# Optimization experiments

Measured on AMD Instinct MI355X. Metric: run time of the kernel, lower is better.

## Reference

```python
import jax, jax.numpy as jnp
import numpy as np

N_NODES, F_IN, HID, HEADS, REP, NCLS = 8192, 128, 64, 8, 512, 32
E, NSYN, LMAX = 2048, 4096, 8
DM, DI, DSTATE, DCONV, DTR = 512, 1024, 16, 4, 32


def setup_inputs():
    key = jax.random.key(0)
    ks = jax.random.split(key, 24)
    g = lambda i, shape, s=0.05: jax.random.normal(ks[i], shape, jnp.float32) * s
    return {
        "edge_attr": jax.random.normal(ks[0], (E, 8), jnp.float32),
        "synapse": jax.random.normal(ks[1], (NSYN, 6), jnp.float32),
        "x_param": g(2, (N_NODES, F_IN), 0.1),
        "W1": g(3, (F_IN, HEADS * HID)),
        "att_src1": g(4, (HEADS, HID), 0.1),
        "att_dst1": g(5, (HEADS, HID), 0.1),
        "b1": jnp.zeros((HEADS * HID,), jnp.float32),
        "W2": g(6, (HEADS * HID, REP)),
        "att_src2": g(7, (1, REP), 0.1),
        "att_dst2": g(8, (1, REP), 0.1),
        "b2": jnp.zeros((REP,), jnp.float32),
        "W_in": g(9, (6, DM), 0.1),
        "b_in": jnp.zeros((DM,), jnp.float32),
        "W_inproj": g(10, (DM, 2 * DI)),
        "conv_w": g(11, (DI, DCONV), 0.1),
        "conv_b": jnp.zeros((DI,), jnp.float32),
        "W_xproj": g(12, (DI, DTR + 2 * DSTATE)),
        "W_dt": g(13, (DTR, DI), 0.1),
        "b_dt": jnp.full((DI,), -4.0, jnp.float32),
        "A_log": jnp.log(jnp.tile(jnp.arange(1, DSTATE + 1, dtype=jnp.float32), (DI, 1))),
        "D": jnp.ones((DI,), jnp.float32),
        "W_outproj": g(14, (DI, DM)),
        "W_lout": g(15, (DM, DM)),
        "b_lout": jnp.zeros((DM,), jnp.float32),
        "Wc1": g(16, (REP + 2 * DM, 512)),
        "bc1": jnp.zeros((512,), jnp.float32),
        "Wc2": g(17, (512, NCLS)),
        "bc2": jnp.zeros((NCLS,), jnp.float32),
        "edge_index": jax.random.randint(ks[18], (2, E), 0, N_NODES),
        "synapse_index": jnp.sort(jax.random.randint(ks[19], (NSYN,), 0, E)),
        "scatter_size": N_NODES,
    }


def _gat(x, W, a_src, a_dst, bias, src, dst, heads, out_ch, concat):
    # PyG GATConv (eval mode, edge_dim=None, self-loops already appended to src/dst)
    n = x.shape[0]
    xw = (x @ W).reshape(n, heads, out_ch)
    e = (xw * a_src).sum(-1)[src] + (xw * a_dst).sum(-1)[dst]  # [E+N, H]
    e = jax.nn.leaky_relu(e, 0.2)
    m = jax.ops.segment_max(e, dst, num_segments=n)
    ex = jnp.exp(e - m[dst])
    denom = jax.ops.segment_sum(ex, dst, num_segments=n)
    alpha = ex / denom[dst]
    out = jax.ops.segment_sum(alpha[:, :, None] * xw[src], dst, num_segments=n)
    out = out.reshape(n, heads * out_ch) if concat else out.mean(1)
    return out + bias


def _mamba_encoder(synapse, synapse_index, W_in, b_in, W_inproj, conv_w, conv_b,
                   W_xproj, W_dt, b_dt, A_log, D, W_outproj, W_lout, b_lout):
    # ragged [NSYN,6] -> padded [E, LMAX, 6] (synapse_index is sorted)
    counts = jax.ops.segment_sum(jnp.ones((NSYN,), jnp.int32), synapse_index, num_segments=E)
    starts = jnp.cumsum(counts) - counts
    pos = jnp.arange(NSYN) - starts[synapse_index]
    padded = jnp.zeros((E, LMAX, synapse.shape[1]), synapse.dtype).at[
        synapse_index, pos].set(synapse, mode="drop")
    u = padded @ W_in + b_in                     # linear_in: [E, L, DM]
    xz = u @ W_inproj                            # in_proj:   [E, L, 2*DI]
    xm, z = xz[..., :DI], xz[..., DI:]
    # depthwise causal conv over time
    xc = jax.lax.conv_general_dilated(
        xm.transpose(0, 2, 1), conv_w[:, None, :],
        window_strides=(1,), padding=[(DCONV - 1, 0)],
        dimension_numbers=("NCH", "OIH", "NCH"), feature_group_count=DI)
    xc = jax.nn.silu(xc + conv_b[:, None]).transpose(0, 2, 1)  # [E, L, DI]
    xdb = xc @ W_xproj
    dt = jax.nn.softplus(xdb[..., :DTR] @ W_dt + b_dt)         # [E, L, DI]
    Bm = xdb[..., DTR:DTR + DSTATE]                            # [E, L, N]
    Cm = xdb[..., DTR + DSTATE:]                               # [E, L, N]
    A = -jnp.exp(A_log)                                        # [DI, N]

    def step(h, t):
        dt_t, B_t, C_t, x_t = t                                # [E,DI],[E,N],[E,N],[E,DI]
        h = jnp.exp(dt_t[:, :, None] * A) * h + (dt_t * x_t)[:, :, None] * B_t[:, None, :]
        return h, jnp.einsum("bdn,bn->bd", h, C_t)

    h0 = jnp.zeros((E, DI, DSTATE), xc.dtype)
    _, ys = jax.lax.scan(step, h0, (dt.transpose(1, 0, 2), Bm.transpose(1, 0, 2),
                                    Cm.transpose(1, 0, 2), xc.transpose(1, 0, 2)))
    y = ys.transpose(1, 0, 2) + D * xc                         # [E, L, DI]
    out = (y * jax.nn.silu(z)) @ W_outproj                     # [E, L, DM]
    # masked mean over true sequence length (empty groups behave like a zero seq of len 1)
    cnt = jnp.clip(counts, 1, LMAX).astype(out.dtype)
    mask = (jnp.arange(LMAX)[None, :] < cnt[:, None]).astype(out.dtype)
    pooled = (out * mask[:, :, None]).sum(1) / cnt[:, None]
    return pooled @ W_lout + b_lout                            # [E, DM]


def _forward(edge_attr, synapse, x_param, W1, att_src1, att_dst1, b1,
             W2, att_src2, att_dst2, b2, W_in, b_in, W_inproj, conv_w, conv_b,
             W_xproj, W_dt, b_dt, A_log, D, W_outproj, W_lout, b_lout,
             Wc1, bc1, Wc2, bc2, edge_index, synapse_index, scatter_size):
    # GAT stack (eval: dropouts identity; edge_attr unused since edge_dim=None)
    loops = jnp.arange(N_NODES)
    src = jnp.concatenate([edge_index[0], loops])
    dst = jnp.concatenate([edge_index[1], loops])
    h = jax.nn.elu(_gat(x_param, W1, att_src1, att_dst1, b1, src, dst, HEADS, HID, True))
    h = _gat(h, W2, att_src2, att_dst2, b2, src, dst, 1, REP, False)   # [N, REP]
    x_point = _mamba_encoder(synapse, synapse_index, W_in, b_in, W_inproj, conv_w,
                             conv_b, W_xproj, W_dt, b_dt, A_log, D, W_outproj,
                             W_lout, b_lout)                            # [E, DM]

    def smax(idx):
        s = jax.ops.segment_max(x_point, idx, num_segments=scatter_size)
        nz = jax.ops.segment_sum(jnp.ones((E,), jnp.int32), idx, num_segments=scatter_size)
        return jnp.where(nz[:, None] > 0, s, 0.0)  # torch_scatter: empty slots -> 0

    left, right = smax(edge_index[0]), smax(edge_index[1])
    feats = jnp.concatenate([h, left, right], axis=1)          # [N, REP+2*DM]
    return jax.nn.relu(feats @ Wc1 + bc1) @ Wc2 + bc2          # [N, NCLS]


def reference(edge_attr, synapse, x_param, W1, att_src1, att_dst1, b1,
              W2, att_src2, att_dst2, b2, W_in, b_in, W_inproj, conv_w, conv_b,
              W_xproj, W_dt, b_dt, A_log, D, W_outproj, W_lout, b_lout,
              Wc1, bc1, Wc2, bc2, edge_index, synapse_index, scatter_size):
    return _forward(edge_attr, synapse, x_param, W1, att_src1, att_dst1, b1,
                    W2, att_src2, att_dst2, b2, W_in, b_in, W_inproj, conv_w, conv_b,
                    W_xproj, W_dt, b_dt, A_log, D, W_outproj, W_lout, b_lout,
                    Wc1, bc1, Wc2, bc2, edge_index, synapse_index, scatter_size)
```

## Files before the change

kernel.cpp:

```cpp
#include <hip/hip_runtime.h>

#define N_NODES 8192
#define F_IN 128
#define HID 64
#define HEADS 8
#define REP 512
#define NCLS 32
#define E_EDGES 2048
#define NSYN 4096
#define LMAX 8
#define DM 512
#define DI 1024
#define DSTATE 16
#define DCONV 4
#define DTR 32
#define TOT_EDGES (E_EDGES + N_NODES)
#define ROWS (E_EDGES * LMAX)
#define MC_CAP 6144

typedef short bf16x8 __attribute__((ext_vector_type(8)));
typedef float f32x4 __attribute__((ext_vector_type(4)));

__device__ __forceinline__ unsigned mapf(float f) {
  unsigned u = __float_as_uint(f);
  return (u & 0x80000000u) ? ~u : (u | 0x80000000u);
}
__device__ __forceinline__ float unmapf(unsigned u) {
  return __uint_as_float((u & 0x80000000u) ? (u ^ 0x80000000u) : ~u);
}
__device__ __forceinline__ float sigmoidf_(float x) { return 1.0f / (1.0f + expf(-x)); }
__device__ __forceinline__ float softplusf_(float x) {
  return fmaxf(x, 0.0f) + log1pf(expf(-fabsf(x)));
}
__device__ __forceinline__ float fsig(float x) {
  return __builtin_amdgcn_rcpf(1.0f + __expf(-x));
}
__device__ __forceinline__ float fsoftplus(float x) {
  return fmaxf(x, 0.0f) + __logf(1.0f + __expf(-fabsf(x)));
}
__device__ __forceinline__ unsigned short f2bf(float f) {
  unsigned u = __float_as_uint(f);
  unsigned r = (u + 0x7FFFu + ((u >> 16) & 1u)) >> 16;
  return (unsigned short)r;
}
__device__ __forceinline__ float bf2f(unsigned short h) {
  return __uint_as_float(((unsigned)h) << 16);
}
__device__ __forceinline__ void split2(float x, unsigned short* hh, unsigned short* ll) {
  unsigned short h = f2bf(x);
  *hh = h;
  *ll = f2bf(x - bf2f(h));
}
__device__ __forceinline__ int lower_bound_dev(const int* __restrict__ arr, int n, int v) {
  int lo = 0, hi = n;
  while (lo < hi) { int mid = (lo + hi) >> 1; if (arr[mid] < v) lo = mid + 1; else hi = mid; }
  return lo;
}
__device__ __forceinline__ int src_of(const int* __restrict__ ei, int i) {
  return i < E_EDGES ? ei[i] : i - E_EDGES;
}
__device__ __forceinline__ int dst_of(const int* __restrict__ ei, int i) {
  return i < E_EDGES ? ei[E_EDGES + i] : i - E_EDGES;
}
__device__ __forceinline__ int clip_cnt(int c) { return c < 1 ? 1 : (c > LMAX ? LMAX : c); }

__global__ __launch_bounds__(256) void gemm_mfma(
    const unsigned short* __restrict__ Ah, const unsigned short* __restrict__ Al,
    const unsigned short* __restrict__ Bth, const unsigned short* __restrict__ Btl,
    float* __restrict__ C, int M, int N, int K,
    const float* __restrict__ bias, int act) {
  __shared__ __align__(16) unsigned short As[2][64][40];
  const int tid = threadIdx.x;
  const int w = tid >> 6;
  const int lane = tid & 63;
  const int brow = blockIdx.y * 64;
  const int bcol = blockIdx.x * 64;
  const int srow = tid >> 2;
  const int skc = tid & 3;
  const int r0 = lane & 15;
  const int kg = lane >> 4;
  f32x4 acc[4] = {};
  const size_t aoff = (size_t)(brow + srow) * K + skc * 8;
  const size_t boff = (size_t)(bcol + w * 16 + r0) * K + kg * 8;
  bf16x8 bh = *(const bf16x8*)(Bth + boff);
  bf16x8 bl = *(const bf16x8*)(Btl + boff);
  *(bf16x8*)(&As[0][srow][skc * 8]) = *(const bf16x8*)(Ah + aoff);
  *(bf16x8*)(&As[1][srow][skc * 8]) = *(const bf16x8*)(Al + aoff);
  __syncthreads();
  for (int kt = 0; kt < K; kt += 32) {
    const bool more = (kt + 32) < K;
    bf16x8 nAh, nAl, nbh, nbl;
    if (more) {
      nAh = *(const bf16x8*)(Ah + aoff + kt + 32);
      nAl = *(const bf16x8*)(Al + aoff + kt + 32);
      nbh = *(const bf16x8*)(Bth + boff + kt + 32);
      nbl = *(const bf16x8*)(Btl + boff + kt + 32);
    }
#pragma unroll
    for (int r = 0; r < 4; ++r) {
      bf16x8 ah = *(const bf16x8*)(&As[0][r * 16 + r0][kg * 8]);
      bf16x8 al = *(const bf16x8*)(&As[1][r * 16 + r0][kg * 8]);
      acc[r] = __builtin_amdgcn_mfma_f32_16x16x32_bf16(ah, bh, acc[r], 0, 0, 0);
      acc[r] = __builtin_amdgcn_mfma_f32_16x16x32_bf16(ah, bl, acc[r], 0, 0, 0);
      acc[r] = __builtin_amdgcn_mfma_f32_16x16x32_bf16(al, bh, acc[r], 0, 0, 0);
    }
    __syncthreads();
    if (more) {
      *(bf16x8*)(&As[0][srow][skc * 8]) = nAh;
      *(bf16x8*)(&As[1][srow][skc * 8]) = nAl;
      bh = nbh; bl = nbl;
    }
    __syncthreads();
  }
  const int col = bcol + w * 16 + r0;
  const float bb = bias ? bias[col] : 0.0f;
#pragma unroll
  for (int r = 0; r < 4; ++r) {
#pragma unroll
    for (int j = 0; j < 4; ++j) {
      int row = brow + r * 16 + kg * 4 + j;
      float v = acc[r][j] + bb;
      if (act == 1) v = fmaxf(v, 0.0f);
      C[(size_t)row * N + col] = v;
    }
  }
}

__global__ __launch_bounds__(256) void gemm_mfma2(
    const unsigned short* __restrict__ Ah, const unsigned short* __restrict__ Al,
    const unsigned short* __restrict__ Bth, const unsigned short* __restrict__ Btl,
    float* __restrict__ C, int M, int N, int K,
    const float* __restrict__ bias, int act) {
  __shared__ __align__(16) unsigned short As[2][128][40];
  __shared__ __align__(16) unsigned short Bs[2][128][40];
  const int tid = threadIdx.x;
  const int w = tid >> 6;
  const int lane = tid & 63;
  const int wr = w >> 1, wc = w & 1;
  const int mb = M >> 7;
  const int lin = blockIdx.x;
  const int bx = lin / mb;
  const int by = lin % mb;
  const int brow = by * 128;
  const int bcol = bx * 128;
  const int r0 = lane & 15;
  const int kg = lane >> 4;
  const int row0 = tid >> 2, kc0 = tid & 3;
  const int row1 = (tid + 256) >> 2, kc1 = (tid + 256) & 3;
  const size_t a0 = (size_t)(brow + row0) * K + kc0 * 8;
  const size_t a1 = (size_t)(brow + row1) * K + kc1 * 8;
  const size_t b0 = (size_t)(bcol + row0) * K + kc0 * 8;
  const size_t b1 = (size_t)(bcol + row1) * K + kc1 * 8;
  f32x4 acc[4][4] = {};
  {
    bf16x8 t0 = *(const bf16x8*)(Ah + a0), t1 = *(const bf16x8*)(Al + a0);
    bf16x8 t2 = *(const bf16x8*)(Bth + b0), t3 = *(const bf16x8*)(Btl + b0);
    bf16x8 t4 = *(const bf16x8*)(Ah + a1), t5 = *(const bf16x8*)(Al + a1);
    bf16x8 t6 = *(const bf16x8*)(Bth + b1), t7 = *(const bf16x8*)(Btl + b1);
    *(bf16x8*)(&As[0][row0][kc0 * 8]) = t0;
    *(bf16x8*)(&As[1][row0][kc0 * 8]) = t1;
    *(bf16x8*)(&Bs[0][row0][kc0 * 8]) = t2;
    *(bf16x8*)(&Bs[1][row0][kc0 * 8]) = t3;
    *(bf16x8*)(&As[0][row1][kc1 * 8]) = t4;
    *(bf16x8*)(&As[1][row1][kc1 * 8]) = t5;
    *(bf16x8*)(&Bs[0][row1][kc1 * 8]) = t6;
    *(bf16x8*)(&Bs[1][row1][kc1 * 8]) = t7;
  }
  __syncthreads();
  for (int kt = 0; kt < K; kt += 32) {
    const bool more = (kt + 32) < K;
    bf16x8 p0, p1, p2, p3, p4, p5, p6, p7;
    if (more) {
      p0 = *(const bf16x8*)(Ah + a0 + kt + 32);
      p1 = *(const bf16x8*)(Al + a0 + kt + 32);
      p2 = *(const bf16x8*)(Bth + b0 + kt + 32);
      p3 = *(const bf16x8*)(Btl + b0 + kt + 32);
      p4 = *(const bf16x8*)(Ah + a1 + kt + 32);
      p5 = *(const bf16x8*)(Al + a1 + kt + 32);
      p6 = *(const bf16x8*)(Bth + b1 + kt + 32);
      p7 = *(const bf16x8*)(Btl + b1 + kt + 32);
    }
    bf16x8 bhv[4], blv[4];
#pragma unroll
    for (int cf = 0; cf < 4; ++cf) {
      bhv[cf] = *(const bf16x8*)(&Bs[0][wc * 64 + cf * 16 + r0][kg * 8]);
      blv[cf] = *(const bf16x8*)(&Bs[1][wc * 64 + cf * 16 + r0][kg * 8]);
    }
#pragma unroll
    for (int rf = 0; rf < 4; ++rf) {
      bf16x8 ah = *(const bf16x8*)(&As[0][wr * 64 + rf * 16 + r0][kg * 8]);
      bf16x8 al = *(const bf16x8*)(&As[1][wr * 64 + rf * 16 + r0][kg * 8]);
#pragma unroll
      for (int cf = 0; cf < 4; ++cf) {
        acc[rf][cf] = __builtin_amdgcn_mfma_f32_16x16x32_bf16(ah, bhv[cf], acc[rf][cf], 0, 0, 0);
        acc[rf][cf] = __builtin_amdgcn_mfma_f32_16x16x32_bf16(ah, blv[cf], acc[rf][cf], 0, 0, 0);
        acc[rf][cf] = __builtin_amdgcn_mfma_f32_16x16x32_bf16(al, bhv[cf], acc[rf][cf], 0, 0, 0);
      }
    }
    __syncthreads();
    if (more) {
      *(bf16x8*)(&As[0][row0][kc0 * 8]) = p0;
      *(bf16x8*)(&As[1][row0][kc0 * 8]) = p1;
      *(bf16x8*)(&Bs[0][row0][kc0 * 8]) = p2;
      *(bf16x8*)(&Bs[1][row0][kc0 * 8]) = p3;
      *(bf16x8*)(&As[0][row1][kc1 * 8]) = p4;
      *(bf16x8*)(&As[1][row1][kc1 * 8]) = p5;
      *(bf16x8*)(&Bs[0][row1][kc1 * 8]) = p6;
      *(bf16x8*)(&Bs[1][row1][kc1 * 8]) = p7;
    }
    __syncthreads();
  }
#pragma unroll
  for (int rf = 0; rf < 4; ++rf)
#pragma unroll
    for (int cf = 0; cf < 4; ++cf) {
      int col = bcol + wc * 64 + cf * 16 + r0;
      float bb = bias ? bias[col] : 0.0f;
#pragma unroll
      for (int j = 0; j < 4; ++j) {
        int row = brow + wr * 64 + rf * 16 + kg * 4 + j;
        float v = acc[rf][cf][j] + bb;
        if (act == 1) v = fmaxf(v, 0.0f);
        C[(size_t)row * N + col] = v;
      }
    }
}

__global__ __launch_bounds__(256) void gemm_mfma_sk(
    const unsigned short* __restrict__ Ah, const unsigned short* __restrict__ Al,
    const unsigned short* __restrict__ Bth, const unsigned short* __restrict__ Btl,
    float* __restrict__ C, int M, int N, int K) {
  __shared__ __align__(16) unsigned short As[2][64][40];
  const int tid = threadIdx.x;
  const int w = tid >> 6;
  const int lane = tid & 63;
  const int brow = blockIdx.y * 64;
  const int bcol = blockIdx.x * 64;
  const int srow = tid >> 2;
  const int skc = tid & 3;
  const int r0 = lane & 15;
  const int kg = lane >> 4;
  const int kchunk = K / gridDim.z;
  const int k0 = blockIdx.z * kchunk;
  f32x4 acc[4] = {};
  const size_t aoff = (size_t)(brow + srow) * K;
  const size_t boff = (size_t)(bcol + w * 16 + r0) * K + kg * 8;
  for (int kt = k0; kt < k0 + kchunk; kt += 32) {
    bf16x8 bh = *(const bf16x8*)(Bth + boff + kt);
    bf16x8 bl = *(const bf16x8*)(Btl + boff + kt);
    *(bf16x8*)(&As[0][srow][skc * 8]) = *(const bf16x8*)(Ah + aoff + kt + skc * 8);
    *(bf16x8*)(&As[1][srow][skc * 8]) = *(const bf16x8*)(Al + aoff + kt + skc * 8);
    __syncthreads();
#pragma unroll
    for (int r = 0; r < 4; ++r) {
      bf16x8 ah = *(const bf16x8*)(&As[0][r * 16 + r0][kg * 8]);
      bf16x8 al = *(const bf16x8*)(&As[1][r * 16 + r0][kg * 8]);
      acc[r] = __builtin_amdgcn_mfma_f32_16x16x32_bf16(ah, bh, acc[r], 0, 0, 0);
      acc[r] = __builtin_amdgcn_mfma_f32_16x16x32_bf16(ah, bl, acc[r], 0, 0, 0);
      acc[r] = __builtin_amdgcn_mfma_f32_16x16x32_bf16(al, bh, acc[r], 0, 0, 0);
    }
    __syncthreads();
  }
  const int col = bcol + w * 16 + r0;
#pragma unroll
  for (int r = 0; r < 4; ++r) {
#pragma unroll
    for (int j = 0; j < 4; ++j) {
      int row = brow + r * 16 + kg * 4 + j;
      atomicAdd(&C[(size_t)row * N + col], acc[r][j]);
    }
  }
}

__global__ void split_kernel(const float* __restrict__ x, unsigned short* __restrict__ h,
                             unsigned short* __restrict__ l, int n) {
  int i = blockIdx.x * 256 + threadIdx.x;
  if (i >= n) return;
  split2(x[i], &h[i], &l[i]);
}

__global__ void tsplit_kernel(const float* __restrict__ W, unsigned short* __restrict__ Wth,
                              unsigned short* __restrict__ Wtl, int K, int N) {
  int i = blockIdx.x * 256 + threadIdx.x;
  if (i >= K * N) return;
  int k = i / N, n = i - k * N;
  float v = W[i];
  unsigned short h = f2bf(v);
  Wth[(size_t)n * K + k] = h;
  Wtl[(size_t)n * K + k] = f2bf(v - bf2f(h));
}

template <int BM, int BN>
__global__ __launch_bounds__(256) void gemm_t(
    const float* __restrict__ A, int lda,
    const float* __restrict__ B, int ldb,
    float* __restrict__ C, int ldc,
    int M, int N, int K,
    const float* __restrict__ bias, int act) {
  constexpr int RR = BM / 64;
  constexpr int CR = BN / 64;
  __shared__ float As[16][BM + 4];
  __shared__ float Bs[16][BN + 4];
  const int tid = threadIdx.x;
  const int tx = tid & 15;
  const int ty = tid >> 4;
  const int brow = blockIdx.y * BM;
  const int bcol = blockIdx.x * BN;
  float acc[RR][CR][4][4] = {};
  for (int kt = 0; kt < K; kt += 16) {
#pragma unroll
    for (int p = 0; p < RR; ++p) {
      int c = tid + p * 256;
      int row = c >> 2, kc = c & 3;
      int gr = brow + row;
      float4 v = make_float4(0.f, 0.f, 0.f, 0.f);
      if (gr < M) v = *reinterpret_cast<const float4*>(A + (size_t)gr * lda + kt + kc * 4);
      As[kc * 4 + 0][row] = v.x;
      As[kc * 4 + 1][row] = v.y;
      As[kc * 4 + 2][row] = v.z;
      As[kc * 4 + 3][row] = v.w;
    }
#pragma unroll
    for (int p = 0; p < CR; ++p) {
      int c = tid + p * 256;
      int k = c / (BN / 4), c4 = c % (BN / 4);
      int gc = bcol + c4 * 4;
      float4 v = make_float4(0.f, 0.f, 0.f, 0.f);
      if (gc < N) v = *reinterpret_cast<const float4*>(B + (size_t)(kt + k) * ldb + gc);
      *reinterpret_cast<float4*>(&Bs[k][c4 * 4]) = v;
    }
    __syncthreads();
#pragma unroll
    for (int k = 0; k < 16; ++k) {
      float av[RR * 4], bv[CR * 4];
#pragma unroll
      for (int r = 0; r < RR; ++r) {
        float4 t = *reinterpret_cast<const float4*>(&As[k][r * 64 + ty * 4]);
        av[r * 4 + 0] = t.x; av[r * 4 + 1] = t.y; av[r * 4 + 2] = t.z; av[r * 4 + 3] = t.w;
      }
#pragma unroll
      for (int cq = 0; cq < CR; ++cq) {
        float4 t = *reinterpret_cast<const float4*>(&Bs[k][cq * 64 + tx * 4]);
        bv[cq * 4 + 0] = t.x; bv[cq * 4 + 1] = t.y; bv[cq * 4 + 2] = t.z; bv[cq * 4 + 3] = t.w;
      }
#pragma unroll
      for (int r = 0; r < RR; ++r)
#pragma unroll
        for (int cq = 0; cq < CR; ++cq)
#pragma unroll
          for (int i = 0; i < 4; ++i)
#pragma unroll
            for (int j = 0; j < 4; ++j)
              acc[r][cq][i][j] = fmaf(av[r * 4 + i], bv[cq * 4 + j], acc[r][cq][i][j]);
    }
    __syncthreads();
  }
#pragma unroll
  for (int r = 0; r < RR; ++r)
#pragma unroll
    for (int i = 0; i < 4; ++i) {
      int row = brow + r * 64 + ty * 4 + i;
      if (row >= M) continue;
#pragma unroll
      for (int cq = 0; cq < CR; ++cq) {
        int col = bcol + cq * 64 + tx * 4;
        if (col >= N) continue;
        float4 v;
        v.x = acc[r][cq][i][0]; v.y = acc[r][cq][i][1];
        v.z = acc[r][cq][i][2]; v.w = acc[r][cq][i][3];
        if (bias) {
          float4 bb = *reinterpret_cast<const float4*>(bias + col);
          v.x += bb.x; v.y += bb.y; v.z += bb.z; v.w += bb.w;
        }
        if (act == 1) {
          v.x = fmaxf(v.x, 0.f); v.y = fmaxf(v.y, 0.f);
          v.z = fmaxf(v.z, 0.f); v.w = fmaxf(v.w, 0.f);
        }
        *reinterpret_cast<float4*>(C + (size_t)row * ldc + col) = v;
      }
    }
}

__global__ void counts_kernel(const int* __restrict__ sidx, int* __restrict__ counts) {
  int e = blockIdx.x * 256 + threadIdx.x;
  if (e >= E_EDGES) return;
  int lo = lower_bound_dev(sidx, NSYN, e);
  int hi = lower_bound_dev(sidx, NSYN, e + 1);
  counts[e] = hi - lo;
}

__global__ void scatter_padded_kernel(const float* __restrict__ synapse,
                                      const int* __restrict__ sidx,
                                      float* __restrict__ padded) {
  int i = blockIdx.x * 256 + threadIdx.x;
  if (i >= NSYN) return;
  int e = sidx[i];
  int lo = lower_bound_dev(sidx, NSYN, e);
  int pos = i - lo;
  if (pos < LMAX) {
#pragma unroll
    for (int c = 0; c < 6; ++c) padded[((size_t)e * LMAX + pos) * 6 + c] = synapse[(size_t)i * 6 + c];
  }
}

__global__ __launch_bounds__(256) void prefix_kernel(const int* __restrict__ counts,
                                                     int* __restrict__ starts_c) {
  __shared__ int part[256];
  int t = threadIdx.x;
  int loc[8];
  int s = 0;
#pragma unroll
  for (int i = 0; i < 8; ++i) {
    int c = clip_cnt(counts[t * 8 + i]);
    loc[i] = s;
    s += c;
  }
  part[t] = s;
  __syncthreads();
  int mytot = s;
  for (int o = 1; o < 256; o <<= 1) {
    int add = (t >= o) ? part[t - o] : 0;
    __syncthreads();
    part[t] += add;
    __syncthreads();
  }
  int off = part[t] - mytot;
#pragma unroll
  for (int i = 0; i < 8; ++i) starts_c[t * 8 + i] = off + loc[i];
}

__global__ __launch_bounds__(256) void xc_compact_kernel(
    const float* __restrict__ padded,
    const float* __restrict__ W_eff, const float* __restrict__ b_eff,
    const float* __restrict__ conv_w, const float* __restrict__ conv_b,
    const int* __restrict__ counts, const int* __restrict__ starts_c,
    unsigned short* __restrict__ xch, unsigned short* __restrict__ xcl) {
  __shared__ float pads[LMAX * 6];
  int t = threadIdx.x;
  int d = blockIdx.x * 256 + t;
  int e = blockIdx.y;
  if (t < LMAX * 6) pads[t] = padded[(size_t)e * LMAX * 6 + t];
  __syncthreads();
  int cnt = clip_cnt(counts[e]);
  int sc = starts_c[e];
  float wef[6];
#pragma unroll
  for (int c = 0; c < 6; ++c) wef[c] = W_eff[c * 2048 + d];
  float cw0 = conv_w[d * 4 + 0], cw1 = conv_w[d * 4 + 1];
  float cw2 = conv_w[d * 4 + 2], cw3 = conv_w[d * 4 + 3];
  float cb = conv_b[d], be = b_eff[d];
  float x0 = 0.f, x1 = 0.f, x2 = 0.f;
  for (int l = 0; l < cnt; ++l) {
    float xm = be;
#pragma unroll
    for (int c = 0; c < 6; ++c) xm += pads[l * 6 + c] * wef[c];
    float s0 = cb + xm * cw3;
    if (l >= 1) s0 += x2 * cw2;
    if (l >= 2) s0 += x1 * cw1;
    if (l >= 3) s0 += x0 * cw0;
    float v = s0 * fsig(s0);
    size_t o = (size_t)(sc + l) * DI + d;
    split2(v, &xch[o], &xcl[o]);
    x0 = x1; x1 = x2; x2 = xm;
  }
}

__global__ __launch_bounds__(256) void mamba_scan_pool_kernel(
    const float* __restrict__ xdb_c, const float* __restrict__ padded,
    const float* __restrict__ W_eff, const float* __restrict__ b_eff,
    const float* __restrict__ W_dt, const float* __restrict__ b_dt,
    const float* __restrict__ A_log, const float* __restrict__ Dv,
    const float* __restrict__ conv_w, const float* __restrict__ conv_b,
    const int* __restrict__ counts, const int* __restrict__ starts_c,
    unsigned short* __restrict__ pooledh, unsigned short* __restrict__ pooledl) {
  __shared__ float pads[LMAX * 6];
  int t = threadIdx.x;
  int d = blockIdx.x * 256 + t;
  int e = blockIdx.y;
  if (t < LMAX * 6) pads[t] = padded[(size_t)e * LMAX * 6 + t];
  float wdt[DTR];
#pragma unroll
  for (int k = 0; k < DTR; ++k) wdt[k] = W_dt[k * DI + d];
  float a[DSTATE];
#pragma unroll
  for (int n = 0; n < DSTATE; ++n) a[n] = -__expf(A_log[d * DSTATE + n]);
  float h[DSTATE];
#pragma unroll
  for (int n = 0; n < DSTATE; ++n) h[n] = 0.0f;
  float wef[6], wez[6];
#pragma unroll
  for (int c = 0; c < 6; ++c) {
    wef[c] = W_eff[c * 2048 + d];
    wez[c] = W_eff[c * 2048 + DI + d];
  }
  float cw0 = conv_w[d * 4 + 0], cw1 = conv_w[d * 4 + 1];
  float cw2 = conv_w[d * 4 + 2], cw3 = conv_w[d * 4 + 3];
  float cb = conv_b[d];
  float bdt = b_dt[d], Dd = Dv[d], be = b_eff[d], bez = b_eff[DI + d];
  __syncthreads();
  int cnt = clip_cnt(counts[e]);
  int sc = starts_c[e];
  float x0 = 0.f, x1 = 0.f, x2 = 0.f;
  float ssum = 0.0f;
  for (int l = 0; l < cnt; ++l) {
    float xm = be;
#pragma unroll
    for (int c = 0; c < 6; ++c) xm += pads[l * 6 + c] * wef[c];
    float s0 = cb + xm * cw3;
    if (l >= 1) s0 += x2 * cw2;
    if (l >= 2) s0 += x1 * cw1;
    if (l >= 3) s0 += x0 * cw0;
    float xt = s0 * fsig(s0);
    const float* __restrict__ xrow = xdb_c + (size_t)(sc + l) * 64;
    float acc = bdt;
#pragma unroll
    for (int k = 0; k < DTR; ++k) acc += xrow[k] * wdt[k];
    float dt = fsoftplus(acc);
    float dtx = dt * xt;
    float y = 0.0f;
#pragma unroll
    for (int n = 0; n < DSTATE; ++n) {
      float en = __expf(dt * a[n]);
      h[n] = en * h[n] + dtx * xrow[32 + n];
      y += h[n] * xrow[48 + n];
    }
    y += Dd * xt;
    float z = bez;
#pragma unroll
    for (int c = 0; c < 6; ++c) z += pads[l * 6 + c] * wez[c];
    ssum += y * z * fsig(z);
    x0 = x1; x1 = x2; x2 = xm;
  }
  float pv = ssum / (float)cnt;
  split2(pv, &pooledh[(size_t)e * DI + d], &pooledl[(size_t)e * DI + d]);
}

__global__ void esed1_kernel(const float* __restrict__ xw1, const float* __restrict__ as1,
                             const float* __restrict__ ad1, float* __restrict__ es1,
                             float* __restrict__ ed1) {
  int idx = blockIdx.x * 256 + threadIdx.x;
  int n = idx >> 3, h = idx & 7;
  const float* xr = xw1 + (size_t)n * 512 + h * 64;
  const float* sr = as1 + h * 64;
  const float* dr = ad1 + h * 64;
  float es = 0.0f, ed = 0.0f;
#pragma unroll
  for (int c = 0; c < 64; ++c) { float v = xr[c]; es += v * sr[c]; ed += v * dr[c]; }
  es1[idx] = es; ed1[idx] = ed;
}

__global__ void edge1_kernel(const int* __restrict__ ei, const float* __restrict__ es1,
                             const float* __restrict__ ed1, float* __restrict__ e1,
                             unsigned* __restrict__ m1u) {
  int idx = blockIdx.x * 256 + threadIdx.x;
  if (idx >= TOT_EDGES * HEADS) return;
  int i = idx >> 3, h = idx & 7;
  int s = src_of(ei, i), d = dst_of(ei, i);
  float v = es1[s * 8 + h] + ed1[d * 8 + h];
  v = v >= 0.0f ? v : 0.2f * v;
  e1[idx] = v;
  atomicMax(m1u + d * 8 + h, mapf(v));
}

__global__ void ex1_kernel(const int* __restrict__ ei, float* __restrict__ e1,
                           const unsigned* __restrict__ m1u, float* __restrict__ denom1) {
  int idx = blockIdx.x * 256 + threadIdx.x;
  if (idx >= TOT_EDGES * HEADS) return;
  int i = idx >> 3, h = idx & 7;
  int d = dst_of(ei, i);
  float ex = expf(e1[idx] - unmapf(m1u[d * 8 + h]));
  e1[idx] = ex;
  atomicAdd(denom1 + d * 8 + h, ex);
}

__global__ __launch_bounds__(256) void agg1_kernel(const int* __restrict__ ei,
                                                   const float* __restrict__ e1,
                                                   const float* __restrict__ denom1,
                                                   const float* __restrict__ xw1,
                                                   float* __restrict__ g1) {
  int i = blockIdx.x;
  int s = src_of(ei, i), d = dst_of(ei, i);
  for (int j = threadIdx.x; j < 512; j += 256) {
    int h = j >> 6;
    float alpha = e1[i * 8 + h] / denom1[d * 8 + h];
    atomicAdd(g1 + (size_t)d * 512 + j, alpha * xw1[(size_t)s * 512 + j]);
  }
}

__global__ void elu_bias_split_kernel(const float* __restrict__ g1, const float* __restrict__ b1,
                                      unsigned short* __restrict__ g1h,
                                      unsigned short* __restrict__ g1l) {
  int idx = blockIdx.x * 256 + threadIdx.x;
  int j = idx & 511;
  float v = g1[idx] + b1[j];
  v = v > 0.0f ? v : expm1f(v);
  split2(v, &g1h[idx], &g1l[idx]);
}

__global__ __launch_bounds__(64) void esed2_kernel(const float* __restrict__ xw2,
                                                   const float* __restrict__ as2,
                                                   const float* __restrict__ ad2,
                                                   float* __restrict__ es2,
                                                   float* __restrict__ ed2) {
  int n = blockIdx.x, t = threadIdx.x;
  float es = 0.0f, ed = 0.0f;
  for (int c = t; c < 512; c += 64) {
    float v = xw2[(size_t)n * 512 + c];
    es += v * as2[c]; ed += v * ad2[c];
  }
#pragma unroll
  for (int o = 32; o > 0; o >>= 1) { es += __shfl_down(es, o, 64); ed += __shfl_down(ed, o, 64); }
  if (t == 0) { es2[n] = es; ed2[n] = ed; }
}

__global__ void edge2_kernel(const int* __restrict__ ei, const float* __restrict__ es2,
                             const float* __restrict__ ed2, float* __restrict__ e2,
                             unsigned* __restrict__ m2u) {
  int i = blockIdx.x * 256 + threadIdx.x;
  if (i >= TOT_EDGES) return;
  int s = src_of(ei, i), d = dst_of(ei, i);
  float v = es2[s] + ed2[d];
  v = v >= 0.0f ? v : 0.2f * v;
  e2[i] = v;
  atomicMax(m2u + d, mapf(v));
}

__global__ void ex2_kernel(const int* __restrict__ ei, float* __restrict__ e2,
                           const unsigned* __restrict__ m2u, float* __restrict__ denom2) {
  int i = blockIdx.x * 256 + threadIdx.x;
  if (i >= TOT_EDGES) return;
  int d = dst_of(ei, i);
  float ex = expf(e2[i] - unmapf(m2u[d]));
  e2[i] = ex;
  atomicAdd(denom2 + d, ex);
}

__global__ __launch_bounds__(256) void agg2_kernel(const int* __restrict__ ei,
                                                   const float* __restrict__ e2,
                                                   const float* __restrict__ denom2,
                                                   const float* __restrict__ xw2,
                                                   float* __restrict__ g2) {
  int i = blockIdx.x;
  int s = src_of(ei, i), d = dst_of(ei, i);
  float alpha = e2[i] / denom2[d];
  for (int j = threadIdx.x; j < 512; j += 256) {
    atomicAdd(g2 + (size_t)d * 512 + j, alpha * xw2[(size_t)s * 512 + j]);
  }
}

__global__ __launch_bounds__(256) void leftright_kernel(const int* __restrict__ ei,
                                                        const float* __restrict__ xp,
                                                        unsigned* __restrict__ leftU,
                                                        unsigned* __restrict__ rightU,
                                                        int* __restrict__ flagL,
                                                        int* __restrict__ flagR) {
  int i = blockIdx.x;
  int s = ei[i], d = ei[E_EDGES + i];
  if (threadIdx.x == 0) { flagL[s] = 1; flagR[d] = 1; }
  for (int j = threadIdx.x; j < 512; j += 256) {
    unsigned v = mapf(xp[(size_t)i * 512 + j]);
    atomicMax(leftU + (size_t)s * 512 + j, v);
    atomicMax(rightU + (size_t)d * 512 + j, v);
  }
}

__global__ void concat_split_kernel(const float* __restrict__ g2, const float* __restrict__ b2,
                                    const unsigned* __restrict__ leftU,
                                    const unsigned* __restrict__ rightU,
                                    const int* __restrict__ flagL, const int* __restrict__ flagR,
                                    unsigned short* __restrict__ fh,
                                    unsigned short* __restrict__ fl) {
  int idx = blockIdx.x * 256 + threadIdx.x;
  int n = idx >> 9, j = idx & 511;
  size_t base = (size_t)n * 1536 + j;
  split2(g2[idx] + b2[j], &fh[base], &fl[base]);
  split2(flagL[n] ? unmapf(leftU[idx]) : 0.0f, &fh[base + 512], &fl[base + 512]);
  split2(flagR[n] ? unmapf(rightU[idx]) : 0.0f, &fh[base + 1024], &fl[base + 1024]);
}

extern "C" void kernel_launch(void* const* d_in, const int* in_sizes, int n_in,
                              void* d_out, int out_size, void* d_ws, size_t ws_size,
                              hipStream_t stream) {
  const float* synapse = (const float*)d_in[1];
  const float* x_param = (const float*)d_in[2];
  const float* W1 = (const float*)d_in[3];
  const float* as1 = (const float*)d_in[4];
  const float* ad1 = (const float*)d_in[5];
  const float* b1 = (const float*)d_in[6];
  const float* W2 = (const float*)d_in[7];
  const float* as2 = (const float*)d_in[8];
  const float* ad2 = (const float*)d_in[9];
  const float* b2 = (const float*)d_in[10];
  const float* W_in = (const float*)d_in[11];
  const float* b_in = (const float*)d_in[12];
  const float* W_inproj = (const float*)d_in[13];
  const float* conv_w = (const float*)d_in[14];
  const float* conv_b = (const float*)d_in[15];
  const float* W_xproj = (const float*)d_in[16];
  const float* W_dt = (const float*)d_in[17];
  const float* b_dt = (const float*)d_in[18];
  const float* A_log = (const float*)d_in[19];
  const float* Dv = (const float*)d_in[20];
  const float* W_outproj = (const float*)d_in[21];
  const float* W_lout = (const float*)d_in[22];
  const float* b_lout = (const float*)d_in[23];
  const float* Wc1 = (const float*)d_in[24];
  const float* bc1 = (const float*)d_in[25];
  const float* Wc2 = (const float*)d_in[26];
  const float* bc2 = (const float*)d_in[27];
  const int* edge_index = (const int*)d_in[28];
  const int* sidx = (const int*)d_in[29];
  float* out = (float*)d_out;

  const size_t MB = (size_t)1 << 20;
  const size_t KB = (size_t)1 << 10;
  char* ws = (char*)d_ws;
  unsigned short* xc_ch = (unsigned short*)(ws + 0);
  unsigned short* xc_cl = (unsigned short*)(ws + 16 * MB);
  float* xw1 = (float*)(ws + 0);
  float* g1 = (float*)(ws + 16 * MB);
  unsigned short* g1h = (unsigned short*)(ws + 32 * MB);
  unsigned short* g1l = (unsigned short*)(ws + 40 * MB);
  unsigned short* xph = (unsigned short*)(ws + 48 * MB);
  unsigned short* xpl = (unsigned short*)(ws + 50 * MB);
  unsigned short* W1th = (unsigned short*)(ws + 52 * MB);
  unsigned short* W1tl = (unsigned short*)(ws + 52 * MB + 128 * KB);
  float* xw2 = (float*)(ws + 48 * MB);
  unsigned short* W2th = (unsigned short*)(ws + 0);
  unsigned short* W2tl = (unsigned short*)(ws + 512 * KB);
  float* g2 = (float*)(ws + 0);
  unsigned short* featsh = (unsigned short*)(ws + 16 * MB);
  unsigned short* featsl = (unsigned short*)(ws + 40 * MB);
  float* hidden = (float*)(ws + 0);
  float* xdb_c = (float*)(ws + 64 * MB);
  unsigned short* pooledh = (unsigned short*)(ws + 68 * MB);
  unsigned short* pooledl = (unsigned short*)(ws + 72 * MB);
  unsigned short* Wxth = (unsigned short*)(ws + 76 * MB);
  unsigned short* Wxtl = (unsigned short*)(ws + 76 * MB + 128 * KB);
  float* Wmix = (float*)(ws + 77 * MB);
  unsigned short* Wmixth = (unsigned short*)(ws + 80 * MB);
  unsigned short* Wmixtl = (unsigned short*)(ws + 81 * MB);
  unsigned* leftU = (unsigned*)(ws + 64 * MB);
  unsigned* rightU = (unsigned*)(ws + 80 * MB);
  float* x_point = (float*)(ws + 96 * MB);
  unsigned short* Wc1th = (unsigned short*)(ws + 96 * MB);
  unsigned short* Wc1tl = (unsigned short*)(ws + 96 * MB + 1536 * KB);
  char* sm = ws + 100 * MB;
  float* es1 = (float*)(sm + 0);
  float* ed1 = (float*)(sm + 256 * KB);
  float* e1 = (float*)(sm + 512 * KB);
  unsigned* m1u = (unsigned*)(sm + 832 * KB);
  float* denom1 = (float*)(sm + 1088 * KB);
  float* es2 = (float*)(sm + 1344 * KB);
  float* ed2 = (float*)(sm + 1376 * KB);
  float* e2 = (float*)(sm + 1408 * KB);
  unsigned* m2u = (unsigned*)(sm + 1448 * KB);
  float* denom2 = (float*)(sm + 1480 * KB);
  int* flagL = (int*)(sm + 1512 * KB);
  int* flagR = (int*)(sm + 1544 * KB);
  float* padded = (float*)(ws + 106 * MB);
  int* counts = (int*)(ws + 106 * MB + 384 * KB);
  float* W_eff = (float*)(ws + 106 * MB + 400 * KB);
  float* b_eff = (float*)(ws + 106 * MB + 448 * KB);
  int* starts_c = (int*)(ws + 106 * MB + 456 * KB);

  auto g64 = [&](const float* A, int lda, const float* B, int ldb, float* C, int ldc,
                 int M, int N, int K, const float* bias, int act) {
    dim3 grid((N + 63) / 64, (M + 63) / 64);
    gemm_t<64, 64><<<grid, 256, 0, stream>>>(A, lda, B, ldb, C, ldc, M, N, K, bias, act);
  };
  auto gm = [&](const unsigned short* Ah, const unsigned short* Al,
                const unsigned short* Bth, const unsigned short* Btl, float* C,
                int M, int N, int K, const float* bias, int act) {
    dim3 grid(N / 64, M / 64);
    gemm_mfma<<<grid, 256, 0, stream>>>(Ah, Al, Bth, Btl, C, M, N, K, bias, act);
  };
  auto gm2 = [&](const unsigned short* Ah, const unsigned short* Al,
                 const unsigned short* Bth, const unsigned short* Btl, float* C,
                 int M, int N, int K, const float* bias, int act) {
    gemm_mfma2<<<(N / 128) * (M / 128), 256, 0, stream>>>(Ah, Al, Bth, Btl, C, M, N, K, bias,
                                                          act);
  };
  auto tsplit = [&](const float* W, unsigned short* th, unsigned short* tl, int K, int N) {
    tsplit_kernel<<<(K * N + 255) / 256, 256, 0, stream>>>(W, th, tl, K, N);
  };

  g64(W_in, DM, W_inproj, 2 * DI, W_eff, 2 * DI, 6, 2 * DI, DM, nullptr, 0);
  g64(b_in, DM, W_inproj, 2 * DI, b_eff, 2 * DI, 1, 2 * DI, DM, nullptr, 0);
  g64(W_outproj, DM, W_lout, DM, Wmix, DM, DI, DM, DM, nullptr, 0);

  hipMemsetAsync(padded, 0, (size_t)ROWS * 6 * 4, stream);
  scatter_padded_kernel<<<(NSYN + 255) / 256, 256, 0, stream>>>(synapse, sidx, padded);
  counts_kernel<<<(E_EDGES + 255) / 256, 256, 0, stream>>>(sidx, counts);
  prefix_kernel<<<1, 256, 0, stream>>>(counts, starts_c);
  xc_compact_kernel<<<dim3(DI / 256, E_EDGES), 256, 0, stream>>>(
      padded, W_eff, b_eff, conv_w, conv_b, counts, starts_c, xc_ch, xc_cl);
  tsplit(W_xproj, Wxth, Wxtl, DI, 64);
  hipMemsetAsync(xdb_c, 0, (size_t)MC_CAP * 64 * 4, stream);
  gemm_mfma_sk<<<dim3(1, MC_CAP / 64, 8), 256, 0, stream>>>(xc_ch, xc_cl, Wxth, Wxtl, xdb_c,
                                                            MC_CAP, 64, DI);
  mamba_scan_pool_kernel<<<dim3(DI / 256, E_EDGES), 256, 0, stream>>>(
      xdb_c, padded, W_eff, b_eff, W_dt, b_dt, A_log, Dv, conv_w, conv_b, counts, starts_c,
      pooledh, pooledl);
  tsplit(Wmix, Wmixth, Wmixtl, DI, DM);
  gm(pooledh, pooledl, Wmixth, Wmixtl, x_point, E_EDGES, DM, DI, b_lout, 0);

  split_kernel<<<(N_NODES * F_IN + 255) / 256, 256, 0, stream>>>(x_param, xph, xpl,
                                                                 N_NODES * F_IN);
  tsplit(W1, W1th, W1tl, F_IN, HEADS * HID);
  gm2(xph, xpl, W1th, W1tl, xw1, N_NODES, HEADS * HID, F_IN, nullptr, 0);
  esed1_kernel<<<(N_NODES * HEADS) / 256, 256, 0, stream>>>(xw1, as1, ad1, es1, ed1);
  hipMemsetAsync(m1u, 0, 512 * KB, stream);
  hipMemsetAsync(g1, 0, (size_t)N_NODES * 512 * 4, stream);
  edge1_kernel<<<(TOT_EDGES * HEADS + 255) / 256, 256, 0, stream>>>(edge_index, es1, ed1, e1, m1u);
  ex1_kernel<<<(TOT_EDGES * HEADS + 255) / 256, 256, 0, stream>>>(edge_index, e1, m1u, denom1);
  agg1_kernel<<<TOT_EDGES, 256, 0, stream>>>(edge_index, e1, denom1, xw1, g1);
  elu_bias_split_kernel<<<(N_NODES * 512) / 256, 256, 0, stream>>>(g1, b1, g1h, g1l);

  tsplit(W2, W2th, W2tl, HEADS * HID, REP);
  gm2(g1h, g1l, W2th, W2tl, xw2, N_NODES, REP, HEADS * HID, nullptr, 0);
  esed2_kernel<<<N_NODES, 64, 0, stream>>>(xw2, as2, ad2, es2, ed2);
  hipMemsetAsync(m2u, 0, 128 * KB, stream);
  hipMemsetAsync(g2, 0, (size_t)N_NODES * 512 * 4, stream);
  edge2_kernel<<<(TOT_EDGES + 255) / 256, 256, 0, stream>>>(edge_index, es2, ed2, e2, m2u);
  ex2_kernel<<<(TOT_EDGES + 255) / 256, 256, 0, stream>>>(edge_index, e2, m2u, denom2);
  agg2_kernel<<<TOT_EDGES, 256, 0, stream>>>(edge_index, e2, denom2, xw2, g2);

  hipMemsetAsync(leftU, 0, 32 * MB, stream);
  leftright_kernel<<<E_EDGES, 256, 0, stream>>>(edge_index, x_point, leftU, rightU, flagL, flagR);

  concat_split_kernel<<<(N_NODES * 512) / 256, 256, 0, stream>>>(g2, b2, leftU, rightU, flagL,
                                                                 flagR, featsh, featsl);
  tsplit(Wc1, Wc1th, Wc1tl, REP + 2 * DM, 512);
  gm2(featsh, featsl, Wc1th, Wc1tl, hidden, N_NODES, 512, REP + 2 * DM, bc1, 1);
  g64(hidden, 512, Wc2, NCLS, out, NCLS, N_NODES, NCLS, 512, bc2, 0);
}
```

Baseline: 486.9 us.

## Replace GAT self-loop atomics with direct init kernels and widen GEMM to 512 threads

The GAT aggregation previously zeroed g1/g2 with a memset and then ran atomic scatter-adds over all edges plus one self-loop per node. Self-loop contributions are now written directly by an elementwise init kernel, so the memset and 8192 blocks of atomics per layer go away and only the real edges use atomicAdd. Separately, the 128x128 MFMA GEMM now runs with 512 threads: each of 8 waves computes a 64x32 sub-tile and each thread loads one chunk instead of two. This cuts per-thread registers and adds waves, at the cost of more LDS reads per MFMA.

```diff
diff --git a/kernel.cpp b/kernel.cpp
--- a/kernel.cpp
+++ b/kernel.cpp
@@ -27,10 +27,6 @@
 }
 __device__ __forceinline__ float unmapf(unsigned u) {
   return __uint_as_float((u & 0x80000000u) ? (u ^ 0x80000000u) : ~u);
-}
-__device__ __forceinline__ float sigmoidf_(float x) { return 1.0f / (1.0f + expf(-x)); }
-__device__ __forceinline__ float softplusf_(float x) {
-  return fmaxf(x, 0.0f) + log1pf(expf(-fabsf(x)));
 }
 __device__ __forceinline__ float fsig(float x) {
   return __builtin_amdgcn_rcpf(1.0f + __expf(-x));
@@ -126,7 +122,7 @@
   }
 }
 
-__global__ __launch_bounds__(256) void gemm_mfma2(
+__global__ __launch_bounds__(512) void gemm_mfma2(
     const unsigned short* __restrict__ Ah, const unsigned short* __restrict__ Al,
     const unsigned short* __restrict__ Bth, const unsigned short* __restrict__ Btl,
     float* __restrict__ C, int M, int N, int K,
@@ -136,7 +132,7 @@
   const int tid = threadIdx.x;
   const int w = tid >> 6;
   const int lane = tid & 63;
-  const int wr = w >> 1, wc = w & 1;
+  const int wr = w >> 2, wc = w & 3;
   const int mb = M >> 7;
   const int lin = blockIdx.x;
   const int bx = lin / mb;
@@ -146,52 +142,39 @@
   const int r0 = lane & 15;
   const int kg = lane >> 4;
   const int row0 = tid >> 2, kc0 = tid & 3;
-  const int row1 = (tid + 256) >> 2, kc1 = (tid + 256) & 3;
   const size_t a0 = (size_t)(brow + row0) * K + kc0 * 8;
-  const size_t a1 = (size_t)(brow + row1) * K + kc1 * 8;
   const size_t b0 = (size_t)(bcol + row0) * K + kc0 * 8;
-  const size_t b1 = (size_t)(bcol + row1) * K + kc1 * 8;
-  f32x4 acc[4][4] = {};
+  f32x4 acc[4][2] = {};
   {
     bf16x8 t0 = *(const bf16x8*)(Ah + a0), t1 = *(const bf16x8*)(Al + a0);
     bf16x8 t2 = *(const bf16x8*)(Bth + b0), t3 = *(const bf16x8*)(Btl + b0);
-    bf16x8 t4 = *(const bf16x8*)(Ah + a1), t5 = *(const bf16x8*)(Al + a1);
-    bf16x8 t6 = *(const bf16x8*)(Bth + b1), t7 = *(const bf16x8*)(Btl + b1);
     *(bf16x8*)(&As[0][row0][kc0 * 8]) = t0;
     *(bf16x8*)(&As[1][row0][kc0 * 8]) = t1;
     *(bf16x8*)(&Bs[0][row0][kc0 * 8]) = t2;
     *(bf16x8*)(&Bs[1][row0][kc0 * 8]) = t3;
-    *(bf16x8*)(&As[0][row1][kc1 * 8]) = t4;
-    *(bf16x8*)(&As[1][row1][kc1 * 8]) = t5;
-    *(bf16x8*)(&Bs[0][row1][kc1 * 8]) = t6;
-    *(bf16x8*)(&Bs[1][row1][kc1 * 8]) = t7;
   }
   __syncthreads();
   for (int kt = 0; kt < K; kt += 32) {
     const bool more = (kt + 32) < K;
-    bf16x8 p0, p1, p2, p3, p4, p5, p6, p7;
+    bf16x8 p0, p1, p2, p3;
     if (more) {
       p0 = *(const bf16x8*)(Ah + a0 + kt + 32);
       p1 = *(const bf16x8*)(Al + a0 + kt + 32);
       p2 = *(const bf16x8*)(Bth + b0 + kt + 32);
       p3 = *(const bf16x8*)(Btl + b0 + kt + 32);
-      p4 = *(const bf16x8*)(Ah + a1 + kt + 32);
-      p5 = *(const bf16x8*)(Al + a1 + kt + 32);
-      p6 = *(const bf16x8*)(Bth + b1 + kt + 32);
-      p7 = *(const bf16x8*)(Btl + b1 + kt + 32);
-    }
-    bf16x8 bhv[4], blv[4];
-#pragma unroll
-    for (int cf = 0; cf < 4; ++cf) {
-      bhv[cf] = *(const bf16x8*)(&Bs[0][wc * 64 + cf * 16 + r0][kg * 8]);
-      blv[cf] = *(const bf16x8*)(&Bs[1][wc * 64 + cf * 16 + r0][kg * 8]);
+    }
+    bf16x8 bhv[2], blv[2];
+#pragma unroll
+    for (int cf = 0; cf < 2; ++cf) {
+      bhv[cf] = *(const bf16x8*)(&Bs[0][wc * 32 + cf * 16 + r0][kg * 8]);
+      blv[cf] = *(const bf16x8*)(&Bs[1][wc * 32 + cf * 16 + r0][kg * 8]);
     }
 #pragma unroll
     for (int rf = 0; rf < 4; ++rf) {
       bf16x8 ah = *(const bf16x8*)(&As[0][wr * 64 + rf * 16 + r0][kg * 8]);
       bf16x8 al = *(const bf16x8*)(&As[1][wr * 64 + rf * 16 + r0][kg * 8]);
 #pragma unroll
-      for (int cf = 0; cf < 4; ++cf) {
+      for (int cf = 0; cf < 2; ++cf) {
         acc[rf][cf] = __builtin_amdgcn_mfma_f32_16x16x32_bf16(ah, bhv[cf], acc[rf][cf], 0, 0, 0);
         acc[rf][cf] = __builtin_amdgcn_mfma_f32_16x16x32_bf16(ah, blv[cf], acc[rf][cf], 0, 0, 0);
         acc[rf][cf] = __builtin_amdgcn_mfma_f32_16x16x32_bf16(al, bhv[cf], acc[rf][cf], 0, 0, 0);
@@ -203,18 +186,14 @@
       *(bf16x8*)(&As[1][row0][kc0 * 8]) = p1;
       *(bf16x8*)(&Bs[0][row0][kc0 * 8]) = p2;
       *(bf16x8*)(&Bs[1][row0][kc0 * 8]) = p3;
-      *(bf16x8*)(&As[0][row1][kc1 * 8]) = p4;
-      *(bf16x8*)(&As[1][row1][kc1 * 8]) = p5;
-      *(bf16x8*)(&Bs[0][row1][kc1 * 8]) = p6;
-      *(bf16x8*)(&Bs[1][row1][kc1 * 8]) = p7;
     }
     __syncthreads();
   }
 #pragma unroll
   for (int rf = 0; rf < 4; ++rf)
 #pragma unroll
-    for (int cf = 0; cf < 4; ++cf) {
-      int col = bcol + wc * 64 + cf * 16 + r0;
+    for (int cf = 0; cf < 2; ++cf) {
+      int col = bcol + wc * 32 + cf * 16 + r0;
       float bb = bias ? bias[col] : 0.0f;
 #pragma unroll
       for (int j = 0; j < 4; ++j) {
@@ -573,13 +552,22 @@
   atomicAdd(denom1 + d * 8 + h, ex);
 }
 
+__global__ void selfinit1_kernel(const float* __restrict__ e1, const float* __restrict__ denom1,
+                                 const float* __restrict__ xw1, float* __restrict__ g1) {
+  int idx = blockIdx.x * 256 + threadIdx.x;
+  int n = idx >> 9, j = idx & 511;
+  int h = j >> 6;
+  float alpha = e1[(size_t)(E_EDGES + n) * 8 + h] / denom1[n * 8 + h];
+  g1[idx] = alpha * xw1[idx];
+}
+
 __global__ __launch_bounds__(256) void agg1_kernel(const int* __restrict__ ei,
                                                    const float* __restrict__ e1,
                                                    const float* __restrict__ denom1,
                                                    const float* __restrict__ xw1,
                                                    float* __restrict__ g1) {
   int i = blockIdx.x;
-  int s = src_of(ei, i), d = dst_of(ei, i);
+  int s = ei[i], d = ei[E_EDGES + i];
   for (int j = threadIdx.x; j < 512; j += 256) {
     int h = j >> 6;
     float alpha = e1[i * 8 + h] / denom1[d * 8 + h];
@@ -635,13 +623,21 @@
   atomicAdd(denom2 + d, ex);
 }
 
+__global__ void selfinit2_kernel(const float* __restrict__ e2, const float* __restrict__ denom2,
+                                 const float* __restrict__ xw2, float* __restrict__ g2) {
+  int idx = blockIdx.x * 256 + threadIdx.x;
+  int n = idx >> 9;
+  float alpha = e2[E_EDGES + n] / denom2[n];
+  g2[idx] = alpha * xw2[idx];
+}
+
 __global__ __launch_bounds__(256) void agg2_kernel(const int* __restrict__ ei,
                                                    const float* __restrict__ e2,
                                                    const float* __restrict__ denom2,
                                                    const float* __restrict__ xw2,
                                                    float* __restrict__ g2) {
   int i = blockIdx.x;
-  int s = src_of(ei, i), d = dst_of(ei, i);
+  int s = ei[i], d = ei[E_EDGES + i];
   float alpha = e2[i] / denom2[d];
   for (int j = threadIdx.x; j < 512; j += 256) {
     atomicAdd(g2 + (size_t)d * 512 + j, alpha * xw2[(size_t)s * 512 + j]);
@@ -778,7 +774,7 @@
   auto gm2 = [&](const unsigned short* Ah, const unsigned short* Al,
                  const unsigned short* Bth, const unsigned short* Btl, float* C,
                  int M, int N, int K, const float* bias, int act) {
-    gemm_mfma2<<<(N / 128) * (M / 128), 256, 0, stream>>>(Ah, Al, Bth, Btl, C, M, N, K, bias,
+    gemm_mfma2<<<(N / 128) * (M / 128), 512, 0, stream>>>(Ah, Al, Bth, Btl, C, M, N, K, bias,
                                                           act);
   };
   auto tsplit = [&](const float* W, unsigned short* th, unsigned short* tl, int K, int N) {
@@ -811,20 +807,20 @@
   gm2(xph, xpl, W1th, W1tl, xw1, N_NODES, HEADS * HID, F_IN, nullptr, 0);
   esed1_kernel<<<(N_NODES * HEADS) / 256, 256, 0, stream>>>(xw1, as1, ad1, es1, ed1);
   hipMemsetAsync(m1u, 0, 512 * KB, stream);
-  hipMemsetAsync(g1, 0, (size_t)N_NODES * 512 * 4, stream);
   edge1_kernel<<<(TOT_EDGES * HEADS + 255) / 256, 256, 0, stream>>>(edge_index, es1, ed1, e1, m1u);
   ex1_kernel<<<(TOT_EDGES * HEADS + 255) / 256, 256, 0, stream>>>(edge_index, e1, m1u, denom1);
-  agg1_kernel<<<TOT_EDGES, 256, 0, stream>>>(edge_index, e1, denom1, xw1, g1);
+  selfinit1_kernel<<<(N_NODES * 512) / 256, 256, 0, stream>>>(e1, denom1, xw1, g1);
+  agg1_kernel<<<E_EDGES, 256, 0, stream>>>(edge_index, e1, denom1, xw1, g1);
   elu_bias_split_kernel<<<(N_NODES * 512) / 256, 256, 0, stream>>>(g1, b1, g1h, g1l);
 
   tsplit(W2, W2th, W2tl, HEADS * HID, REP);
   gm2(g1h, g1l, W2th, W2tl, xw2, N_NODES, REP, HEADS * HID, nullptr, 0);
   esed2_kernel<<<N_NODES, 64, 0, stream>>>(xw2, as2, ad2, es2, ed2);
   hipMemsetAsync(m2u, 0, 128 * KB, stream);
-  hipMemsetAsync(g2, 0, (size_t)N_NODES * 512 * 4, stream);
   edge2_kernel<<<(TOT_EDGES + 255) / 256, 256, 0, stream>>>(edge_index, es2, ed2, e2, m2u);
   ex2_kernel<<<(TOT_EDGES + 255) / 256, 256, 0, stream>>>(edge_index, e2, m2u, denom2);
-  agg2_kernel<<<TOT_EDGES, 256, 0, stream>>>(edge_index, e2, denom2, xw2, g2);
+  selfinit2_kernel<<<(N_NODES * 512) / 256, 256, 0, stream>>>(e2, denom2, xw2, g2);
+  agg2_kernel<<<E_EDGES, 256, 0, stream>>>(edge_index, e2, denom2, xw2, g2);
 
   hipMemsetAsync(leftU, 0, 32 * MB, stream);
   leftright_kernel<<<E_EDGES, 256, 0, stream>>>(edge_index, x_point, leftU, rightU, flagL, flagR);
```

Measured after the change: 454.5 us. 6.7% less time.
